# Kernel optimization log

Hardware: AMD Instinct MI355X
Metric: run time of the kernel (lower is better)

## Reference

```python
import jax, jax.numpy as jnp
import numpy as np

S = 2048        # q_len == context_length
HID = 4096      # hidden_size
NH = 32         # num_attention_heads
NKV = 8         # num_key_value_heads
HD = HID // NH  # head_dim = 128
THETA = 10000.0


def setup_inputs() -> dict:
    key = jax.random.key(0)
    ks = jax.random.split(key, 5)
    hidden_states = jax.random.normal(ks[0], (1, S, HID), dtype=jnp.float32)
    # 1x1 Conv2d weights == linear weights (out_ch, in_ch)
    wq = jax.random.normal(ks[1], (NH * HD, HID), dtype=jnp.float32) * 0.02
    wk = jax.random.normal(ks[2], (NKV * HD, HID), dtype=jnp.float32) * 0.02
    wv = jax.random.normal(ks[3], (NKV * HD, HID), dtype=jnp.float32) * 0.02
    wo = jax.random.normal(ks[4], (HID, NH * HD), dtype=jnp.float32) * 0.02
    # RoPE tables: rotate() only ever uses the first half_dim of cos/sin,
    # so build (1,1,S,half) directly (equivalent to cat(freqs,freqs) then slice).
    half = HD // 2
    inv_freq = 1.0 / (THETA ** (jnp.arange(0, HD, 2, dtype=jnp.float32) / HD))
    freqs = jnp.outer(jnp.arange(S, dtype=jnp.float32), inv_freq)  # (S, half)
    cos = jnp.cos(freqs)[None, None]  # (1,1,S,half)
    sin = jnp.sin(freqs)[None, None]
    # additive causal mask (1,1,S,S): 0 on/below diagonal, large negative above
    causal_mask = jnp.where(
        jnp.arange(S)[:, None] >= jnp.arange(S)[None, :], 0.0, -1e9
    ).astype(jnp.float32)[None, None]
    return dict(hidden_states=hidden_states, wq=wq, wk=wk, wv=wv, wo=wo,
                cos=cos, sin=sin, causal_mask=causal_mask)


def _rope(x, cos, sin):
    # x: (H, S, D); cos/sin: (1,1,S,D/2)
    half = x.shape[-1] // 2
    x1, x2 = x[..., :half], x[..., half:]
    c, s = cos[0, 0], sin[0, 0]  # (S, half), broadcasts over heads
    return jnp.concatenate([x1 * c - x2 * s, x2 * c + x1 * s], axis=-1)


def reference(hidden_states, wq, wk, wv, wo, cos, sin, causal_mask):
    x = hidden_states[0]               # (S, HID); bsz hard-coded to 1 in source
    seq = x.shape[0]
    # 1x1 conv projections == matmul; channel layout is head-major (h*HD + d)
    q = (x @ wq.T).reshape(seq, NH, HD).transpose(1, 0, 2)    # (NH, S, D)
    k = (x @ wk.T).reshape(seq, NKV, HD).transpose(1, 0, 2)   # (NKV, S, D)
    v = (x @ wv.T).reshape(seq, NKV, HD).transpose(1, 0, 2)   # (NKV, S, D)
    q = _rope(q, cos, sin)
    k = _rope(k, cos, sin)
    # repeat_kv: unsqueeze(1).repeat(n_rep).view -> head idx = rep*NKV + kv == tile
    n_rep = NH // NKV
    k = jnp.tile(k, (n_rep, 1, 1))     # (NH, S, D)
    v = jnp.tile(v, (n_rep, 1, 1))
    scale = 1.0 / np.sqrt(HD).astype(np.float32)
    scores = jnp.einsum('hqd,hkd->hqk', q, k) * scale + causal_mask[0, 0]
    attn = jax.nn.softmax(scores, axis=-1)                    # == ANE_softmax
    out = jnp.einsum('hqk,hkd->hqd', attn, v)                 # (NH, S, D)
    out = out.transpose(1, 0, 2).reshape(seq, NH * HD)        # (S, HID)
    return (out @ wo.T)[None]                                 # (1, S, HID)
```

## Files before the change

### kernel.cpp

```cpp
#include <hip/hip_runtime.h>
#include <hip/hip_bf16.h>

#define S_LEN 2048
#define HID   4096
#define NH    32
#define NKV   8
#define HD    128
#define QKV_N 6144
#define KDIM  4096

typedef __attribute__((ext_vector_type(8))) short short8;
typedef __attribute__((ext_vector_type(4))) float floatx4;
typedef unsigned short ushort;

__device__ __forceinline__ unsigned short f2bu(float f) {
  __hip_bfloat16 b = __float2bfloat16(f);
  return *reinterpret_cast<unsigned short*>(&b);
}
__device__ __forceinline__ void store_c(float* p, float v) { *p = v; }
__device__ __forceinline__ void store_c(__hip_bfloat16* p, float v) { *p = __float2bfloat16(v); }

__device__ __forceinline__ void async_copy16(const void* g, void* l) {
  __builtin_amdgcn_global_load_lds((const __attribute__((address_space(1))) void*)g,
                                   (__attribute__((address_space(3))) void*)l, 16, 0, 0);
}

struct bf16x4 { __hip_bfloat16 a, b, c, d; };
__global__ void cvt_f32_bf16(const float* __restrict__ src, __hip_bfloat16* __restrict__ dst, int n4) {
  int i = blockIdx.x * blockDim.x + threadIdx.x;
  if (i < n4) {
    float4 v = ((const float4*)src)[i];
    bf16x4 o = { __float2bfloat16(v.x), __float2bfloat16(v.y),
                 __float2bfloat16(v.z), __float2bfloat16(v.w) };
    ((bf16x4*)dst)[i] = o;
  }
}

template <typename CT>
__global__ __launch_bounds__(256, 2) void gemm_nt(const __hip_bfloat16* __restrict__ A,
                                                  const __hip_bfloat16* __restrict__ B,
                                                  CT* __restrict__ C, int M, int N, int K) {
  __shared__ __align__(16) ushort As[128 * 64];
  __shared__ __align__(16) ushort Bs[128 * 64];
  const int tid  = threadIdx.x;
  const int bm   = blockIdx.y * 128;
  const int bn   = blockIdx.x * 128;
  const int wave = tid >> 6;
  const int lane = tid & 63;
  const int ww   = (wave >> 1) * 64;
  const int wc   = (wave & 1) * 64;
  const int l15  = lane & 15;
  const int quad = lane >> 4;

  const ushort* Au = (const ushort*)A;
  const ushort* Bu = (const ushort*)B;

  const int rr  = lane >> 3;
  const int cc  = lane & 7;
  const int gch = cc ^ rr;
  const ushort* Ag = Au + (size_t)(bm + wave * 32 + rr) * K + gch * 8;
  const ushort* Bg = Bu + (size_t)(bn + wave * 32 + rr) * K + gch * 8;

  floatx4 acc[4][4] = {};

  for (int k0 = 0; k0 < K; k0 += 64) {
    __syncthreads();
#pragma unroll
    for (int e = 0; e < 4; ++e) {
      async_copy16(Ag + (size_t)(e * 8) * K + k0, &As[(wave * 32 + e * 8) * 64]);
      async_copy16(Bg + (size_t)(e * 8) * K + k0, &Bs[(wave * 32 + e * 8) * 64]);
    }
    __syncthreads();
#pragma unroll
    for (int kd = 0; kd < 2; ++kd) {
      short8 af[4], bf[4];
#pragma unroll
      for (int i = 0; i < 4; ++i) {
        af[i] = *(const short8*)&As[(ww + i * 16 + l15) * 64 + ((kd * 4 + quad) ^ (l15 & 7)) * 8];
        bf[i] = *(const short8*)&Bs[(wc + i * 16 + l15) * 64 + ((kd * 4 + quad) ^ (l15 & 7)) * 8];
      }
#pragma unroll
      for (int mi = 0; mi < 4; ++mi)
#pragma unroll
        for (int ni = 0; ni < 4; ++ni)
          acc[mi][ni] = __builtin_amdgcn_mfma_f32_16x16x32_bf16(af[mi], bf[ni], acc[mi][ni], 0, 0, 0);
    }
  }
#pragma unroll
  for (int mi = 0; mi < 4; ++mi)
#pragma unroll
    for (int ni = 0; ni < 4; ++ni)
#pragma unroll
      for (int r = 0; r < 4; ++r) {
        int row = bm + ww + mi * 16 + quad * 4 + r;
        int col = bn + wc + ni * 16 + l15;
        store_c(&C[(size_t)row * N + col], acc[mi][ni][r]);
      }
}

__global__ void rope_qk(const __hip_bfloat16* __restrict__ QKV,
                        const float* __restrict__ cosp, const float* __restrict__ sinp,
                        __hip_bfloat16* __restrict__ Qh, __hip_bfloat16* __restrict__ Kh) {
  int s = blockIdx.y;
  int col = blockIdx.x * 256 + threadIdx.x;
  if (col >= 5120) return;
  const size_t base = (size_t)s * QKV_N;
  float x = __bfloat162float(QKV[base + col]);
  int dd = col & 127;
  float val;
  if (dd < 64) {
    float xp = __bfloat162float(QKV[base + col + 64]);
    val = x * cosp[s * 64 + dd] - xp * sinp[s * 64 + dd];
  } else {
    int f = dd - 64;
    float xp = __bfloat162float(QKV[base + col - 64]);
    val = x * cosp[s * 64 + f] + xp * sinp[s * 64 + f];
  }
  if (col < HID) {
    int h = col >> 7;
    Qh[((size_t)h * S_LEN + s) * HD + dd] = __float2bfloat16(val * 0.08838834764831845f);
  } else {
    int h = (col - HID) >> 7;
    Kh[((size_t)h * S_LEN + s) * HD + dd] = __float2bfloat16(val);
  }
}

__global__ void v_transpose(const __hip_bfloat16* __restrict__ QKV, __hip_bfloat16* __restrict__ Vt) {
  __shared__ ushort tile[64][130];
  int h = blockIdx.y;
  int s0 = blockIdx.x * 64;
  int t = threadIdx.x;
  const ushort* src = (const ushort*)QKV;
#pragma unroll
  for (int i = 0; i < 32; ++i) {
    int flat = i * 256 + t;
    int r = flat >> 7, c = flat & 127;
    tile[r][c] = src[(size_t)(s0 + r) * QKV_N + 5120 + h * 128 + c];
  }
  __syncthreads();
  ushort* dst = (ushort*)Vt;
#pragma unroll
  for (int i = 0; i < 8; ++i) {
    int g = i * 256 + t;
    int d = g >> 4, j4 = (g & 15) * 4;
    ushort4 o;
    o.x = tile[j4][d]; o.y = tile[j4 + 1][d]; o.z = tile[j4 + 2][d]; o.w = tile[j4 + 3][d];
    *(ushort4*)&dst[((size_t)h * HD + d) * S_LEN + s0 + j4] = o;
  }
}

__global__ __launch_bounds__(128, 2) void attn(const __hip_bfloat16* __restrict__ Qh,
                                               const __hip_bfloat16* __restrict__ Kh,
                                               const __hip_bfloat16* __restrict__ Vt,
                                               __hip_bfloat16* __restrict__ AO) {
  __shared__ __align__(16) ushort Ks[64][128];
  __shared__ __align__(16) ushort P[2][32][72];
  const int bi   = blockIdx.x;
  const int g    = bi >> 8;
  const int c    = bi & 255;
  const int head = c & 31;
  const int u    = c >> 5;
  const int t    = (g == 0) ? (24 + u) : (g == 1) ? (16 + u)
                 : (g == 2) ? (15 - u) : (7 - u);
  const int wave = threadIdx.x >> 6;
  const int lane = threadIdx.x & 63;
  const int l15 = lane & 15, quad = lane >> 4;
  const int hk = head & 7;
  const int q0 = t * 64 + wave * 32;
  const ushort* Qu = (const ushort*)Qh + (size_t)head * S_LEN * HD;
  const ushort* Ku = (const ushort*)Kh + (size_t)hk * S_LEN * HD;
  const ushort* Vu = (const ushort*)Vt + (size_t)hk * HD * S_LEN;

  const int rr4  = lane >> 4;
  const int cc16 = lane & 15;
  auto stage = [&](int j0) {
#pragma unroll
    for (int e = 0; e < 8; ++e) {
      int rt = (e * 4 + rr4) & 15;
      int gc = cc16 ^ rt;
      async_copy16(Ku + (size_t)(j0 + wave * 32 + e * 4 + rr4) * HD + gc * 8,
                   &Ks[wave * 32 + e * 4][0]);
    }
  };

  short8 qf[2][4];
#pragma unroll
  for (int mt = 0; mt < 2; ++mt)
#pragma unroll
    for (int kd = 0; kd < 4; ++kd)
      qf[mt][kd] = *(const short8*)(Qu + (size_t)(q0 + mt * 16 + l15) * HD + kd * 32 + quad * 8);

  floatx4 o[2][8] = {};
  float mst[2], lsum[2];
  mst[0] = mst[1] = -1e30f;
  lsum[0] = lsum[1] = 0.f;
  const int nsteps = t + 1;

  stage(0);
  for (int s = 0; s < nsteps; ++s) {
    const int j0 = s * 64;
    __syncthreads();

    floatx4 sc[2][4];
#pragma unroll
    for (int mt = 0; mt < 2; ++mt)
#pragma unroll
      for (int nt = 0; nt < 4; ++nt) sc[mt][nt] = floatx4{0.f, 0.f, 0.f, 0.f};
    __builtin_amdgcn_s_setprio(1);
#pragma unroll
    for (int nt = 0; nt < 4; ++nt) {
      short8 kf[4];
#pragma unroll
      for (int kd = 0; kd < 4; ++kd)
        kf[kd] = *(const short8*)&Ks[nt * 16 + l15][((kd * 4 + quad) ^ l15) * 8];
#pragma unroll
      for (int mt = 0; mt < 2; ++mt)
#pragma unroll
        for (int kd = 0; kd < 4; ++kd)
          sc[mt][nt] = __builtin_amdgcn_mfma_f32_16x16x32_bf16(kf[kd], qf[mt][kd], sc[mt][nt], 0, 0, 0);
    }
    __builtin_amdgcn_s_setprio(0);
    __syncthreads();
    if (s + 1 < nsteps) stage(j0 + 64);

    short8 vf0[8];
#pragma unroll
    for (int t8 = 0; t8 < 8; ++t8)
      vf0[t8] = *(const short8*)(Vu + (size_t)(t8 * 16 + l15) * S_LEN + j0 + quad * 8);

    const bool diag = (s == t);
#pragma unroll
    for (int mt = 0; mt < 2; ++mt) {
      const int qloc = wave * 32 + mt * 16 + l15;
      float pv[16];
      float vmloc = -1e30f;
#pragma unroll
      for (int nt = 0; nt < 4; ++nt)
#pragma unroll
        for (int r = 0; r < 4; ++r) {
          float x = sc[mt][nt][r];
          if (diag && (nt * 16 + quad * 4 + r > qloc)) x = -1e30f;
          pv[nt * 4 + r] = x;
          vmloc = fmaxf(vmloc, x);
        }
      float vm = fmaxf(vmloc, __shfl_xor(vmloc, 16));
      vm = fmaxf(vm, __shfl_xor(vm, 32));
      float ps = 0.f;
      ushort pk[16];
#pragma unroll
      for (int i = 0; i < 16; ++i) {
        float p = __expf(pv[i] - mst[mt]);
        ps += p;
        pk[i] = f2bu(p);
      }
      if (__any(vm > mst[mt] + 8.0f)) {
        const float mnew = fmaxf(mst[mt], vm);
        const float al = __expf(mst[mt] - mnew);
        mst[mt] = mnew;
        lsum[mt] *= al;
        ps = 0.f;
#pragma unroll
        for (int i = 0; i < 16; ++i) {
          float p = __expf(pv[i] - mst[mt]);
          ps += p;
          pk[i] = f2bu(p);
        }
        float ar[4];
#pragma unroll
        for (int r = 0; r < 4; ++r)
          ar[r] = __shfl(al, (lane & 48) | (quad * 4 + r));
#pragma unroll
        for (int t8 = 0; t8 < 8; ++t8)
#pragma unroll
          for (int r = 0; r < 4; ++r) o[mt][t8][r] *= ar[r];
      }
      lsum[mt] += ps;
#pragma unroll
      for (int nt = 0; nt < 4; ++nt) {
        ushort4 w;
        w.x = pk[nt * 4 + 0]; w.y = pk[nt * 4 + 1];
        w.z = pk[nt * 4 + 2]; w.w = pk[nt * 4 + 3];
        *(ushort4*)&P[wave][mt * 16 + l15][nt * 16 + quad * 4] = w;
      }
    }

    short8 vf1[8];
#pragma unroll
    for (int t8 = 0; t8 < 8; ++t8)
      vf1[t8] = *(const short8*)(Vu + (size_t)(t8 * 16 + l15) * S_LEN + j0 + 32 + quad * 8);

    asm volatile("s_waitcnt lgkmcnt(0)" ::: "memory");
    short8 pf[2][2];
#pragma unroll
    for (int mt = 0; mt < 2; ++mt)
#pragma unroll
      for (int hh = 0; hh < 2; ++hh)
        pf[mt][hh] = *(const short8*)&P[wave][mt * 16 + l15][hh * 32 + quad * 8];
    __builtin_amdgcn_s_setprio(1);
#pragma unroll
    for (int t8 = 0; t8 < 8; ++t8)
#pragma unroll
      for (int mt = 0; mt < 2; ++mt) {
        o[mt][t8] = __builtin_amdgcn_mfma_f32_16x16x32_bf16(pf[mt][0], vf0[t8], o[mt][t8], 0, 0, 0);
        o[mt][t8] = __builtin_amdgcn_mfma_f32_16x16x32_bf16(pf[mt][1], vf1[t8], o[mt][t8], 0, 0, 0);
      }
    __builtin_amdgcn_s_setprio(0);
  }

#pragma unroll
  for (int mt = 0; mt < 2; ++mt) {
    float ls = lsum[mt];
    ls += __shfl_xor(ls, 16);
    ls += __shfl_xor(ls, 32);
    float inv[4];
#pragma unroll
    for (int r = 0; r < 4; ++r)
      inv[r] = 1.0f / __shfl(ls, (lane & 48) | (quad * 4 + r));
#pragma unroll
    for (int r = 0; r < 4; ++r) {
      const int row = q0 + mt * 16 + quad * 4 + r;
#pragma unroll
      for (int t8 = 0; t8 < 8; ++t8)
        AO[(size_t)row * HID + head * HD + t8 * 16 + l15] = __float2bfloat16(o[mt][t8][r] * inv[r]);
    }
  }
}

extern "C" void kernel_launch(void* const* d_in, const int* in_sizes, int n_in,
                              void* d_out, int out_size, void* d_ws, size_t ws_size,
                              hipStream_t stream) {
  const float* x    = (const float*)d_in[0];
  const float* wq   = (const float*)d_in[1];
  const float* wk   = (const float*)d_in[2];
  const float* wv   = (const float*)d_in[3];
  const float* wo   = (const float*)d_in[4];
  const float* cosp = (const float*)d_in[5];
  const float* sinp = (const float*)d_in[6];
  float* out = (float*)d_out;

  char* ws = (char*)d_ws;
  size_t off = 0;
  auto alloc = [&](size_t bytes) { char* p = ws + off; off += (bytes + 255) & ~255ull; return p; };
  __hip_bfloat16* Xb   = (__hip_bfloat16*)alloc((size_t)S_LEN * KDIM * 2);
  __hip_bfloat16* Wqkv = (__hip_bfloat16*)alloc((size_t)QKV_N * KDIM * 2);
  __hip_bfloat16* Wob  = (__hip_bfloat16*)alloc((size_t)HID * HID * 2);
  __hip_bfloat16* QKVb = (__hip_bfloat16*)alloc((size_t)S_LEN * QKV_N * 2);
  __hip_bfloat16* Qh   = (__hip_bfloat16*)alloc((size_t)NH * S_LEN * HD * 2);
  __hip_bfloat16* Kh   = (__hip_bfloat16*)alloc((size_t)NKV * S_LEN * HD * 2);
  __hip_bfloat16* Vt   = (__hip_bfloat16*)alloc((size_t)NKV * HD * S_LEN * 2);
  __hip_bfloat16* AO   = (__hip_bfloat16*)alloc((size_t)S_LEN * HID * 2);

  auto cvt = [&](const float* s, __hip_bfloat16* dpt, size_t n) {
    int n4 = (int)(n / 4);
    cvt_f32_bf16<<<dim3((n4 + 255) / 256), dim3(256), 0, stream>>>(s, dpt, n4);
  };
  cvt(x, Xb, (size_t)S_LEN * KDIM);
  cvt(wq, Wqkv, (size_t)HID * KDIM);
  cvt(wk, Wqkv + (size_t)HID * KDIM, (size_t)NKV * HD * KDIM);
  cvt(wv, Wqkv + (size_t)(HID + NKV * HD) * KDIM, (size_t)NKV * HD * KDIM);
  cvt(wo, Wob, (size_t)HID * HID);

  gemm_nt<__hip_bfloat16><<<dim3(QKV_N / 128, S_LEN / 128), dim3(256), 0, stream>>>(
      Xb, Wqkv, QKVb, S_LEN, QKV_N, KDIM);
  rope_qk<<<dim3(20, S_LEN), dim3(256), 0, stream>>>(QKVb, cosp, sinp, Qh, Kh);
  v_transpose<<<dim3(S_LEN / 64, NKV), dim3(256), 0, stream>>>(QKVb, Vt);
  attn<<<dim3(1024), dim3(128), 0, stream>>>(Qh, Kh, Vt, AO);
  gemm_nt<float><<<dim3(HID / 128, S_LEN / 128), dim3(256), 0, stream>>>(
      AO, Wob, out, S_LEN, HID, KDIM);
}
```

Baseline: 529.7 us.

## Use 256x256 pipelined QKV GEMM and merge f32-to-bf16 conversions into one kernel

Adds a new 512-thread QKV projection GEMM with 256x256 tiles. It double-buffers LDS via async global-to-LDS loads, uses explicit waitcnt/barrier phases, raises MFMA priority with setprio, and remaps workgroups into XCD-friendly groups. The goal is to hide load latency and improve operand reuse over the old 128x128 kernel. The five separate conversion launches become one grid-stride kernel, cutting launch overhead. The hand-written sync schedule is fragile, and the larger tiles give only 192 workgroups, which may underfill the GPU.

New measurement: 577.2 us. 9.0% more time.

```diff
diff --git a/kernel.cpp b/kernel.cpp
--- a/kernel.cpp
+++ b/kernel.cpp
@@ -25,14 +25,33 @@
                                    (__attribute__((address_space(3))) void*)l, 16, 0, 0);
 }
 
+#define LGKM0  asm volatile("s_waitcnt lgkmcnt(0)" ::: "memory")
+#define VMC4   asm volatile("s_waitcnt vmcnt(4)" ::: "memory")
+#define VMC0   asm volatile("s_waitcnt vmcnt(0)" ::: "memory")
+#define PH_BAR __builtin_amdgcn_s_barrier()
+
 struct bf16x4 { __hip_bfloat16 a, b, c, d; };
-__global__ void cvt_f32_bf16(const float* __restrict__ src, __hip_bfloat16* __restrict__ dst, int n4) {
-  int i = blockIdx.x * blockDim.x + threadIdx.x;
-  if (i < n4) {
-    float4 v = ((const float4*)src)[i];
+__global__ void cvt_all(const float* __restrict__ x,  const float* __restrict__ wq,
+                        const float* __restrict__ wk, const float* __restrict__ wv,
+                        const float* __restrict__ wo,
+                        __hip_bfloat16* __restrict__ Xb, __hip_bfloat16* __restrict__ Wqkv,
+                        __hip_bfloat16* __restrict__ Wob) {
+  const int S0 = 2097152;
+  const int S1 = 6291456;
+  const int S2 = 7340032;
+  const int S3 = 8388608;
+  const int S4 = 12582912;
+  for (int i = blockIdx.x * blockDim.x + threadIdx.x; i < S4; i += gridDim.x * blockDim.x) {
+    float4 v;
+    bf16x4* d;
+    if (i < S0)      { v = ((const float4*)x)[i];        d = (bf16x4*)Xb + i; }
+    else if (i < S1) { v = ((const float4*)wq)[i - S0];  d = (bf16x4*)Wqkv + (i - S0); }
+    else if (i < S2) { v = ((const float4*)wk)[i - S1];  d = (bf16x4*)Wqkv + (i - S0); }
+    else if (i < S3) { v = ((const float4*)wv)[i - S2];  d = (bf16x4*)Wqkv + (i - S0); }
+    else             { v = ((const float4*)wo)[i - S3];  d = (bf16x4*)Wob + (i - S3); }
     bf16x4 o = { __float2bfloat16(v.x), __float2bfloat16(v.y),
                  __float2bfloat16(v.z), __float2bfloat16(v.w) };
-    ((bf16x4*)dst)[i] = o;
+    *d = o;
   }
 }
 
@@ -95,6 +114,139 @@
         int row = bm + ww + mi * 16 + quad * 4 + r;
         int col = bn + wc + ni * 16 + l15;
         store_c(&C[(size_t)row * N + col], acc[mi][ni][r]);
+      }
+}
+
+__global__ __launch_bounds__(512, 2) void gemm_nt_256(const __hip_bfloat16* __restrict__ A,
+                                                      const __hip_bfloat16* __restrict__ B,
+                                                      __hip_bfloat16* __restrict__ C,
+                                                      int M, int N, int K) {
+  __shared__ __align__(16) ushort As[2][2][128 * 64];
+  __shared__ __align__(16) ushort Bs[2][2][128 * 64];
+  const int tid  = threadIdx.x;
+  const int wv_  = tid >> 6;
+  const int lane = tid & 63;
+  const int l15  = lane & 15;
+  const int quad = lane >> 4;
+  const int wm   = wv_ >> 2;
+  const int wn   = wv_ & 3;
+
+  const int nwg = gridDim.x;
+  const int cpx = nwg >> 3;
+  const int f   = (blockIdx.x & 7) * cpx + (blockIdx.x >> 3);
+  const int nbx = N >> 8;
+  const int bm  = (f / nbx) << 8;
+  const int bn  = (f % nbx) << 8;
+
+  const ushort* Au = (const ushort*)A;
+  const ushort* Bu = (const ushort*)B;
+
+  auto stageA = [&](int slot, int half, int kt) {
+#pragma unroll
+    for (int e = 0; e < 2; ++e) {
+      int n = e * 512 + wv_ * 64 + lane;
+      int row = n >> 3, gc = (n & 7) ^ ((n >> 3) & 7);
+      async_copy16(Au + (size_t)(bm + half * 128 + row) * K + kt * 64 + gc * 8,
+                   &As[slot][half][(e * 512 + wv_ * 64) * 8]);
+    }
+  };
+  auto stageB = [&](int slot, int half, int kt) {
+#pragma unroll
+    for (int e = 0; e < 2; ++e) {
+      int n = e * 512 + wv_ * 64 + lane;
+      int row = n >> 3, gc = (n & 7) ^ ((n >> 3) & 7);
+      async_copy16(Bu + (size_t)(bn + half * 128 + row) * K + kt * 64 + gc * 8,
+                   &Bs[slot][half][(e * 512 + wv_ * 64) * 8]);
+    }
+  };
+
+  floatx4 acc[8][4] = {};
+  short8 a[4][2], b[4][2];
+
+#define LDA(SLOT, I0)                                                                       \
+  {                                                                                         \
+    _Pragma("unroll") for (int ii = 0; ii < 4; ++ii) _Pragma("unroll") for (int kd = 0; kd < 2; ++kd) \
+        a[ii][kd] = *(const short8*)&As[SLOT][wm][((I0) * 16 + ii * 16 + l15) * 64 +        \
+                                                  (((kd * 4 + quad) ^ (l15 & 7)) * 8)];     \
+  }
+#define LDB(SLOT, J0)                                                                       \
+  {                                                                                         \
+    _Pragma("unroll") for (int jj = 0; jj < 2; ++jj) _Pragma("unroll") for (int kd = 0; kd < 2; ++kd) \
+        b[(J0) + jj][kd] = *(const short8*)&Bs[SLOT][wn >> 1][((wn & 1) * 64 + ((J0) + jj) * 16 + l15) * 64 + \
+                                                              (((kd * 4 + quad) ^ (l15 & 7)) * 8)]; \
+  }
+#define MM(IA, JB)                                                                          \
+  {                                                                                         \
+    __builtin_amdgcn_s_setprio(1);                                                          \
+    _Pragma("unroll") for (int ii = 0; ii < 4; ++ii)                                        \
+    _Pragma("unroll") for (int jj = 0; jj < 2; ++jj)                                        \
+    _Pragma("unroll") for (int kd = 0; kd < 2; ++kd)                                        \
+        acc[(IA) + ii][(JB) + jj] = __builtin_amdgcn_mfma_f32_16x16x32_bf16(                \
+            a[ii][kd], b[(JB) + jj][kd], acc[(IA) + ii][(JB) + jj], 0, 0, 0);               \
+    __builtin_amdgcn_s_setprio(0);                                                          \
+  }
+
+  stageA(0, 0, 0); stageA(0, 1, 0); stageB(0, 0, 0); stageB(0, 1, 0);
+  stageB(1, 0, 1); stageB(1, 1, 1);
+  VMC4;
+  PH_BAR;
+
+  const int NI = K >> 7;
+  for (int it = 0; it < NI; ++it) {
+    const int kt0 = 2 * it;
+    const bool pre = (it + 1 < NI);
+    LDA(0, 0); LDB(0, 0);
+    stageA(1, 0, kt0 + 1);
+    PH_BAR; LGKM0;
+    MM(0, 0);
+    PH_BAR;
+    LDB(0, 2);
+    stageA(1, 1, kt0 + 1);
+    PH_BAR; LGKM0;
+    MM(0, 2);
+    PH_BAR;
+    LDA(0, 4);
+    if (pre) stageB(0, 0, kt0 + 2);
+    PH_BAR; LGKM0;
+    MM(4, 0);
+    PH_BAR;
+    if (pre) { stageB(0, 1, kt0 + 2); VMC4; } else { VMC0; }
+    PH_BAR;
+    MM(4, 2);
+    PH_BAR;
+    LDA(1, 0); LDB(1, 0);
+    if (pre) stageA(0, 0, kt0 + 2);
+    PH_BAR; LGKM0;
+    MM(0, 0);
+    PH_BAR;
+    LDB(1, 2);
+    if (pre) stageA(0, 1, kt0 + 2);
+    PH_BAR; LGKM0;
+    MM(0, 2);
+    PH_BAR;
+    LDA(1, 4);
+    if (pre) stageB(1, 0, kt0 + 3);
+    PH_BAR; LGKM0;
+    MM(4, 0);
+    PH_BAR;
+    if (pre) { stageB(1, 1, kt0 + 3); VMC4; } else { VMC0; }
+    PH_BAR;
+    MM(4, 2);
+    PH_BAR;
+  }
+#undef LDA
+#undef LDB
+#undef MM
+
+#pragma unroll
+  for (int i = 0; i < 8; ++i)
+#pragma unroll
+    for (int j = 0; j < 4; ++j)
+#pragma unroll
+      for (int r = 0; r < 4; ++r) {
+        int row = bm + wm * 128 + i * 16 + quad * 4 + r;
+        int col = bn + wn * 64 + j * 16 + l15;
+        C[(size_t)row * N + col] = __float2bfloat16(acc[i][j][r]);
       }
 }
 
@@ -350,17 +502,9 @@
   __hip_bfloat16* Vt   = (__hip_bfloat16*)alloc((size_t)NKV * HD * S_LEN * 2);
   __hip_bfloat16* AO   = (__hip_bfloat16*)alloc((size_t)S_LEN * HID * 2);
 
-  auto cvt = [&](const float* s, __hip_bfloat16* dpt, size_t n) {
-    int n4 = (int)(n / 4);
-    cvt_f32_bf16<<<dim3((n4 + 255) / 256), dim3(256), 0, stream>>>(s, dpt, n4);
-  };
-  cvt(x, Xb, (size_t)S_LEN * KDIM);
-  cvt(wq, Wqkv, (size_t)HID * KDIM);
-  cvt(wk, Wqkv + (size_t)HID * KDIM, (size_t)NKV * HD * KDIM);
-  cvt(wv, Wqkv + (size_t)(HID + NKV * HD) * KDIM, (size_t)NKV * HD * KDIM);
-  cvt(wo, Wob, (size_t)HID * HID);
-
-  gemm_nt<__hip_bfloat16><<<dim3(QKV_N / 128, S_LEN / 128), dim3(256), 0, stream>>>(
+  cvt_all<<<dim3(3072), dim3(256), 0, stream>>>(x, wq, wk, wv, wo, Xb, Wqkv, Wob);
+
+  gemm_nt_256<<<dim3((QKV_N / 256) * (S_LEN / 256)), dim3(512), 0, stream>>>(
       Xb, Wqkv, QKVb, S_LEN, QKV_N, KDIM);
   rope_qk<<<dim3(20, S_LEN), dim3(256), 0, stream>>>(QKVb, cosp, sinp, Qh, Kh);
   v_transpose<<<dim3(S_LEN / 64, NKV), dim3(256), 0, stream>>>(QKVb, Vt);
```
